# Performance work log

Hardware: AMD Instinct MI355X
Metric: run time of the kernel (lower is better)

Reference implementation:

```python
import jax, jax.numpy as jnp
import numpy as np

N_NODES = 50000
N_EDGES = 800000
N_GRAPHS = 512
IN_CH, HID_CH, OUT_CH, N_CLASSES = 128, 64, 64, 10


def gcn_conv(x, src, dst, ew, W, b, n_nodes):
    """PyG GCNConv: add self-loops (weight 1), symmetric normalization, x @ W, scatter-add at dst, + bias."""
    xw = x @ W  # [N, out]
    loop = jnp.arange(n_nodes, dtype=src.dtype)
    src_f = jnp.concatenate([src, loop])
    dst_f = jnp.concatenate([dst, loop])
    ew_f = jnp.concatenate([ew, jnp.ones((n_nodes,), dtype=ew.dtype)])
    deg = jax.ops.segment_sum(ew_f, dst_f, num_segments=n_nodes)  # [N]
    dinv = jnp.where(deg > 0, jax.lax.rsqrt(deg), 0.0)
    norm = dinv[src_f] * ew_f * dinv[dst_f]  # [E+N]
    msg = norm[:, None] * xw[src_f]  # gather + scale
    out = jax.ops.segment_sum(msg, dst_f, num_segments=n_nodes)  # scatter-add
    return out + b


def setup_inputs() -> dict:
    key = jax.random.key(0)
    ks = jax.random.split(key, 12)
    x = jax.random.normal(ks[0], (N_NODES, IN_CH), dtype=jnp.float32)
    edge_index = jax.random.randint(ks[1], (2, N_EDGES), 0, N_NODES, dtype=jnp.int64)
    edge_attr = jax.random.uniform(ks[2], (N_EDGES,), dtype=jnp.float32)
    batch = jnp.sort(jax.random.randint(ks[3], (N_NODES,), 0, N_GRAPHS, dtype=jnp.int64))
    def glorot(k, shape):
        lim = np.sqrt(6.0 / (shape[0] + shape[1]))
        return jax.random.uniform(k, shape, jnp.float32, -lim, lim)
    W1 = glorot(ks[4], (IN_CH, HID_CH))
    b1 = jnp.zeros((HID_CH,), jnp.float32)
    W2 = glorot(ks[5], (HID_CH, OUT_CH))
    b2 = jnp.zeros((OUT_CH,), jnp.float32)
    LW1 = glorot(ks[6], (OUT_CH, 32))
    Lb1 = jnp.zeros((32,), jnp.float32)
    LW2 = glorot(ks[7], (32, N_CLASSES))
    Lb2 = jnp.zeros((N_CLASSES,), jnp.float32)
    return {"x": x, "edge_index": edge_index, "edge_attr": edge_attr, "batch": batch,
            "W1": W1, "b1": b1, "W2": W2, "b2": b2,
            "LW1": LW1, "Lb1": Lb1, "LW2": LW2, "Lb2": Lb2}


def reference(x, edge_index, edge_attr, batch, W1, b1, W2, b2, LW1, Lb1, LW2, Lb2):
    src, dst = edge_index[0], edge_index[1]
    h = gcn_conv(x, src, dst, edge_attr, W1, b1, N_NODES)
    h = jax.nn.relu(h)
    h = gcn_conv(h, src, dst, edge_attr, W2, b2, N_NODES)
    # global mean pool over graphs
    sums = jax.ops.segment_sum(h, batch, num_segments=N_GRAPHS)  # [G, OUT]
    cnt = jax.ops.segment_sum(jnp.ones((N_NODES,), h.dtype), batch, num_segments=N_GRAPHS)
    pooled = sums / jnp.maximum(cnt, 1.0)[:, None]
    # head (dropout treated as identity for deterministic reference)
    h1 = pooled @ LW1 + Lb1
    return h1 @ LW2 + Lb2
```

## Files before the change

kernel.cpp:

```cpp
#include <hip/hip_runtime.h>
#include <hip/hip_bf16.h>

static constexpr int NN = 50000;
static constexpr int NE = 800000;
static constexpr int NG = 512;
static constexpr int NB = 196;


__global__ void zero_kernel(float* __restrict__ p, int n) {
    int i = blockIdx.x * blockDim.x + threadIdx.x;
    if (i < n) p[i] = 0.f;
}

__global__ void hist64_kernel(const int* __restrict__ dst, const float* __restrict__ ew,
                              unsigned long long* __restrict__ h, int* __restrict__ rank) {
    int e = blockIdx.x * blockDim.x + threadIdx.x;
    if (e >= NE) return;
    int d = dst[e];
    unsigned int fx = __float2uint_rn(ew[e] * 1048576.0f);
    unsigned long long pack = (1ULL << 40) | (unsigned long long)fx;
    unsigned long long old = atomicAdd(&h[d], pack);
    rank[e] = (int)(old >> 40);
}

__global__ void dinv_kernel(const unsigned long long* __restrict__ h,
                            float* __restrict__ dinv) {
    int i = blockIdx.x * blockDim.x + threadIdx.x;
    if (i < NN) {
        float deg = (float)(h[i] & ((1ULL << 40) - 1)) * (1.0f / 1048576.0f) + 1.0f;
        dinv[i] = 1.0f / sqrtf(deg);
    }
}


__device__ __forceinline__ int block_scan_inclusive(int v, int* wtot) {
    int lane = threadIdx.x & 63, wid = threadIdx.x >> 6;
    int inc = v;
#pragma unroll
    for (int off = 1; off < 64; off <<= 1) {
        int n = __shfl_up(inc, (unsigned)off, 64);
        if (lane >= off) inc += n;
    }
    if (lane == 63) wtot[wid] = inc;
    __syncthreads();
    int add = 0;
    for (int w = 0; w < wid; ++w) add += wtot[w];
    return inc + add;
}

__global__ __launch_bounds__(256) void scanA_kernel(const unsigned long long* __restrict__ h,
                                                    int* __restrict__ partial) {
    int i = blockIdx.x * 256 + threadIdx.x;
    int v = (i < NN) ? (int)(h[i] >> 40) : 0;
    __shared__ int wsum[4];
    int lane = threadIdx.x & 63, wid = threadIdx.x >> 6;
#pragma unroll
    for (int off = 32; off > 0; off >>= 1) v += __shfl_down(v, (unsigned)off, 64);
    if (lane == 0) wsum[wid] = v;
    __syncthreads();
    if (threadIdx.x == 0) partial[blockIdx.x] = wsum[0] + wsum[1] + wsum[2] + wsum[3];
}

__global__ __launch_bounds__(256) void scanB_kernel(const int* __restrict__ partial,
                                                    int* __restrict__ poff) {
    __shared__ int wtot[4];
    int t = threadIdx.x;
    int v = (t < NB) ? partial[t] : 0;
    int incl = block_scan_inclusive(v, wtot);
    if (t < NB) poff[t] = incl - v;
}

__global__ __launch_bounds__(256) void scanC_kernel(const unsigned long long* __restrict__ h,
                                                    const int* __restrict__ poff,
                                                    int* __restrict__ rowptr) {
    __shared__ int wtot[4];
    int i = blockIdx.x * 256 + threadIdx.x;
    int v = (i < NN) ? (int)(h[i] >> 40) : 0;
    int incl = block_scan_inclusive(v, wtot);
    if (i < NN) rowptr[i + 1] = poff[blockIdx.x] + incl;
    if (i == 0) rowptr[0] = 0;
}

__global__ void scatter_kernel(const int* __restrict__ src, const int* __restrict__ dst,
                               const float* __restrict__ ew, const float* __restrict__ dinv,
                               const int* __restrict__ rowptr, const int* __restrict__ rank,
                               int2* __restrict__ epack) {
    int e = blockIdx.x * blockDim.x + threadIdx.x;
    if (e >= NE) return;
    int s = src[e], d = dst[e];
    int pos = rowptr[d] + rank[e];
    float coef = dinv[s] * ew[e] * dinv[d];
    epack[pos] = make_int2(s, __float_as_int(coef));
}

__global__ void bounds_kernel(const int* __restrict__ batch, int* __restrict__ gbeg,
                              int* __restrict__ gend) {
    int i = blockIdx.x * blockDim.x + threadIdx.x;
    if (i >= NN) return;
    int g = batch[i];
    if (i == 0 || batch[i - 1] != g) gbeg[g] = i;
    if (i == NN - 1 || batch[i + 1] != g) gend[g] = i + 1;
}

template <int K>
__global__ __launch_bounds__(256) void gemm_kernel(const float* __restrict__ X,
                                                   const float* __restrict__ W,
                                                   ushort* __restrict__ out) {
    __shared__ float Xs[64][68];
    __shared__ float Ws[K][64];
    for (int i = threadIdx.x; i < K * 16; i += 256)
        ((float4*)Ws)[i] = ((const float4*)W)[i];
    int tx = threadIdx.x & 15, ty = threadIdx.x >> 4;
    int row0 = blockIdx.x * 64;
    float acc[4][4] = {};
    for (int kb = 0; kb < K; kb += 64) {
        __syncthreads();
        for (int i = threadIdx.x; i < 1024; i += 256) {
            int r = i >> 4, k4 = i & 15;
            int gr = row0 + r; if (gr >= NN) gr = NN - 1;
            float4 v = *(const float4*)(X + (long long)gr * K + kb + k4 * 4);
            *(float4*)&Xs[r][k4 * 4] = v;
        }
        __syncthreads();
#pragma unroll 16
        for (int k = 0; k < 64; ++k) {
            float4 wv = *(const float4*)&Ws[kb + k][tx * 4];
            float x0 = Xs[ty * 4 + 0][k];
            float x1 = Xs[ty * 4 + 1][k];
            float x2 = Xs[ty * 4 + 2][k];
            float x3 = Xs[ty * 4 + 3][k];
            acc[0][0] = fmaf(x0, wv.x, acc[0][0]); acc[0][1] = fmaf(x0, wv.y, acc[0][1]);
            acc[0][2] = fmaf(x0, wv.z, acc[0][2]); acc[0][3] = fmaf(x0, wv.w, acc[0][3]);
            acc[1][0] = fmaf(x1, wv.x, acc[1][0]); acc[1][1] = fmaf(x1, wv.y, acc[1][1]);
            acc[1][2] = fmaf(x1, wv.z, acc[1][2]); acc[1][3] = fmaf(x1, wv.w, acc[1][3]);
            acc[2][0] = fmaf(x2, wv.x, acc[2][0]); acc[2][1] = fmaf(x2, wv.y, acc[2][1]);
            acc[2][2] = fmaf(x2, wv.z, acc[2][2]); acc[2][3] = fmaf(x2, wv.w, acc[2][3]);
            acc[3][0] = fmaf(x3, wv.x, acc[3][0]); acc[3][1] = fmaf(x3, wv.y, acc[3][1]);
            acc[3][2] = fmaf(x3, wv.z, acc[3][2]); acc[3][3] = fmaf(x3, wv.w, acc[3][3]);
        }
    }
#pragma unroll
    for (int j = 0; j < 4; ++j) {
        int r = row0 + ty * 4 + j;
        if (r < NN) {
            ushort4 sv;
            sv.x = __hip_bfloat16_raw(__float2bfloat16(acc[j][0])).x;
            sv.y = __hip_bfloat16_raw(__float2bfloat16(acc[j][1])).x;
            sv.z = __hip_bfloat16_raw(__float2bfloat16(acc[j][2])).x;
            sv.w = __hip_bfloat16_raw(__float2bfloat16(acc[j][3])).x;
            *(ushort4*)(out + (long long)r * 64 + tx * 4) = sv;
        }
    }
}

__device__ __forceinline__ float bf16_ld(const ushort* p) {
    return __uint_as_float((unsigned)(*p) << 16);
}

template <bool RELU>
__global__ __launch_bounds__(256) void agg_kernel(const ushort* __restrict__ xw,
                                                  const int* __restrict__ rowptr,
                                                  const int2* __restrict__ epack,
                                                  const float* __restrict__ dinv,
                                                  const float* __restrict__ bias,
                                                  float* __restrict__ out) {
    int node = blockIdx.x * 4 + (threadIdx.x >> 6);
    int c = threadIdx.x & 63;
    if (node >= NN) return;
    float di = dinv[node];
    float acc = fmaf(di * di, bf16_ld(xw + node * 64 + c), bias[c]);
    float acc2 = 0.f;
    int j = rowptr[node], end = rowptr[node + 1];
    for (; j + 3 < end; j += 4) {
        int2 p0 = epack[j];
        int2 p1 = epack[j + 1];
        int2 p2 = epack[j + 2];
        int2 p3 = epack[j + 3];
        float v0 = bf16_ld(xw + p0.x * 64 + c);
        float v1 = bf16_ld(xw + p1.x * 64 + c);
        float v2 = bf16_ld(xw + p2.x * 64 + c);
        float v3 = bf16_ld(xw + p3.x * 64 + c);
        acc  = fmaf(__int_as_float(p0.y), v0, acc);
        acc2 = fmaf(__int_as_float(p1.y), v1, acc2);
        acc  = fmaf(__int_as_float(p2.y), v2, acc);
        acc2 = fmaf(__int_as_float(p3.y), v3, acc2);
    }
    for (; j < end; ++j) {
        int2 p0 = epack[j];
        acc = fmaf(__int_as_float(p0.y), bf16_ld(xw + p0.x * 64 + c), acc);
    }
    acc += acc2;
    if (RELU) acc = fmaxf(acc, 0.f);
    out[node * 64 + c] = acc;
}

__global__ __launch_bounds__(256) void poolhead_kernel(const float* __restrict__ h,
                                                       const int* __restrict__ gbeg,
                                                       const int* __restrict__ gend,
                                                       const float* __restrict__ LW1,
                                                       const float* __restrict__ Lb1,
                                                       const float* __restrict__ LW2,
                                                       const float* __restrict__ Lb2,
                                                       float* __restrict__ out) {
    __shared__ float pp[4][64];
    __shared__ float p[64];
    __shared__ float t1[32];
    int g = blockIdx.x, t = threadIdx.x;
    int lane = t & 63, wid = t >> 6;
    int b = gbeg[g], e = gend[g];
    float acc = 0.f;
    for (int i = b + wid; i < e; i += 4) acc += h[i * 64 + lane];
    pp[wid][lane] = acc;
    __syncthreads();
    if (t < 64) {
        float s = pp[0][t] + pp[1][t] + pp[2][t] + pp[3][t];
        p[t] = s / fmaxf((float)(e - b), 1.0f);
    }
    __syncthreads();
    if (t < 32) {
        float a = Lb1[t];
#pragma unroll
        for (int k = 0; k < 64; ++k) a = fmaf(p[k], LW1[k * 32 + t], a);
        t1[t] = a;
    }
    __syncthreads();
    if (t < 10) {
        float a = Lb2[t];
#pragma unroll
        for (int j = 0; j < 32; ++j) a = fmaf(t1[j], LW2[j * 10 + t], a);
        out[g * 10 + t] = a;
    }
}


extern "C" void kernel_launch(void* const* d_in, const int* in_sizes, int n_in,
                              void* d_out, int out_size, void* d_ws, size_t ws_size,
                              hipStream_t stream) {
    const float* x     = (const float*)d_in[0];
    const int*   ei    = (const int*)d_in[1];
    const float* ew    = (const float*)d_in[2];
    const int*   batch = (const int*)d_in[3];
    const float* W1    = (const float*)d_in[4];
    const float* b1    = (const float*)d_in[5];
    const float* W2    = (const float*)d_in[6];
    const float* b2    = (const float*)d_in[7];
    const float* LW1   = (const float*)d_in[8];
    const float* Lb1   = (const float*)d_in[9];
    const float* LW2   = (const float*)d_in[10];
    const float* Lb2   = (const float*)d_in[11];

    const int* src = ei;
    const int* dst = ei + NE;

    float* ws = (float*)d_ws;
    unsigned long long* h64 = (unsigned long long*)ws;
    int*   gbeg   = (int*)(ws + 100096);
    int*   gend   = (int*)(ws + 100608);
    float* dinv   = ws + 101120;
    int*   rowptr = (int*)(ws + 151168);
    int*   partial  = (int*)(ws + 201216);
    int*   poff     = (int*)(ws + 201472);
    int2*  epack  = (int2*)(ws + 201728);
    ushort* bufA  = (ushort*)(ws + 1801728);
    float* bufB   = ws + 5001728;
    int*   rank   = (int*)(ws + 5001728);

    zero_kernel<<<(101120 + 255) / 256, 256, 0, stream>>>(ws, 101120);

    hist64_kernel<<<(NE + 255) / 256, 256, 0, stream>>>(dst, ew, h64, rank);
    dinv_kernel<<<NB, 256, 0, stream>>>(h64, dinv);
    scanA_kernel<<<NB, 256, 0, stream>>>(h64, partial);
    scanB_kernel<<<1, 256, 0, stream>>>(partial, poff);
    scanC_kernel<<<NB, 256, 0, stream>>>(h64, poff, rowptr);
    scatter_kernel<<<(NE + 255) / 256, 256, 0, stream>>>(src, dst, ew, dinv, rowptr, rank, epack);
    bounds_kernel<<<NB, 256, 0, stream>>>(batch, gbeg, gend);

    gemm_kernel<128><<<(NN + 63) / 64, 256, 0, stream>>>(x, W1, bufA);
    agg_kernel<true><<<(NN + 3) / 4, 256, 0, stream>>>(bufA, rowptr, epack, dinv, b1, bufB);

    gemm_kernel<64><<<(NN + 63) / 64, 256, 0, stream>>>(bufB, W2, bufA);
    agg_kernel<false><<<(NN + 3) / 4, 256, 0, stream>>>(bufA, rowptr, epack, dinv, b2, bufB);

    poolhead_kernel<<<NG, 256, 0, stream>>>(bufB, gbeg, gend, LW1, Lb1, LW2, Lb2, (float*)d_out);
}
```

Measured before the change: 275.9 us.

## Fuse setup kernels, store hidden layer in bf16, vectorize aggregation across edge halves

Merges the dinv and scanA kernels, and folds the graph-bounds computation into scanC, cutting two launches. The hidden activation after layer 1 is now stored as bf16, and the second GEMM gets a bf16-input load path, halving that intermediate's traffic. The aggregation kernel now has each lane handle two channels via ushort2 loads, with the two half-waves processing alternating edges and combining through a shuffle. The dst-side dinv factor moves out of the per-edge coefficient into a single multiply per node. The extra bf16 rounding of the hidden layer adds precision loss, and half the lanes sit idle during the output writes.

```diff
diff --git a/kernel.cpp b/kernel.cpp
--- a/kernel.cpp
+++ b/kernel.cpp
@@ -5,6 +5,13 @@
 static constexpr int NE = 800000;
 static constexpr int NG = 512;
 static constexpr int NB = 196;
+
+__device__ __forceinline__ float bfu(ushort u) {
+    return __uint_as_float((unsigned)u << 16);
+}
+__device__ __forceinline__ ushort fbf(float f) {
+    return __hip_bfloat16_raw(__float2bfloat16(f)).x;
+}
 
 
 __global__ void zero_kernel(float* __restrict__ p, int n) {
@@ -23,15 +30,26 @@
     rank[e] = (int)(old >> 40);
 }
 
-__global__ void dinv_kernel(const unsigned long long* __restrict__ h,
-                            float* __restrict__ dinv) {
-    int i = blockIdx.x * blockDim.x + threadIdx.x;
+__global__ __launch_bounds__(256) void dinv_scanA_kernel(const unsigned long long* __restrict__ h,
+                                                         float* __restrict__ dinv,
+                                                         int* __restrict__ partial) {
+    int i = blockIdx.x * 256 + threadIdx.x;
+    int cnt = 0;
     if (i < NN) {
-        float deg = (float)(h[i] & ((1ULL << 40) - 1)) * (1.0f / 1048576.0f) + 1.0f;
+        unsigned long long v = h[i];
+        cnt = (int)(v >> 40);
+        float deg = (float)(v & ((1ULL << 40) - 1)) * (1.0f / 1048576.0f) + 1.0f;
         dinv[i] = 1.0f / sqrtf(deg);
     }
-}
-
+    __shared__ int wsum[4];
+    int lane = threadIdx.x & 63, wid = threadIdx.x >> 6;
+    int v = cnt;
+#pragma unroll
+    for (int off = 32; off > 0; off >>= 1) v += __shfl_down(v, (unsigned)off, 64);
+    if (lane == 0) wsum[wid] = v;
+    __syncthreads();
+    if (threadIdx.x == 0) partial[blockIdx.x] = wsum[0] + wsum[1] + wsum[2] + wsum[3];
+}
 
 __device__ __forceinline__ int block_scan_inclusive(int v, int* wtot) {
     int lane = threadIdx.x & 63, wid = threadIdx.x >> 6;
@@ -46,19 +64,6 @@
     int add = 0;
     for (int w = 0; w < wid; ++w) add += wtot[w];
     return inc + add;
-}
-
-__global__ __launch_bounds__(256) void scanA_kernel(const unsigned long long* __restrict__ h,
-                                                    int* __restrict__ partial) {
-    int i = blockIdx.x * 256 + threadIdx.x;
-    int v = (i < NN) ? (int)(h[i] >> 40) : 0;
-    __shared__ int wsum[4];
-    int lane = threadIdx.x & 63, wid = threadIdx.x >> 6;
-#pragma unroll
-    for (int off = 32; off > 0; off >>= 1) v += __shfl_down(v, (unsigned)off, 64);
-    if (lane == 0) wsum[wid] = v;
-    __syncthreads();
-    if (threadIdx.x == 0) partial[blockIdx.x] = wsum[0] + wsum[1] + wsum[2] + wsum[3];
 }
 
 __global__ __launch_bounds__(256) void scanB_kernel(const int* __restrict__ partial,
@@ -70,14 +75,22 @@
     if (t < NB) poff[t] = incl - v;
 }
 
-__global__ __launch_bounds__(256) void scanC_kernel(const unsigned long long* __restrict__ h,
-                                                    const int* __restrict__ poff,
-                                                    int* __restrict__ rowptr) {
+__global__ __launch_bounds__(256) void scanC_bounds_kernel(const unsigned long long* __restrict__ h,
+                                                           const int* __restrict__ poff,
+                                                           int* __restrict__ rowptr,
+                                                           const int* __restrict__ batch,
+                                                           int* __restrict__ gbeg,
+                                                           int* __restrict__ gend) {
     __shared__ int wtot[4];
     int i = blockIdx.x * 256 + threadIdx.x;
     int v = (i < NN) ? (int)(h[i] >> 40) : 0;
     int incl = block_scan_inclusive(v, wtot);
-    if (i < NN) rowptr[i + 1] = poff[blockIdx.x] + incl;
+    if (i < NN) {
+        rowptr[i + 1] = poff[blockIdx.x] + incl;
+        int g = batch[i];
+        if (i == 0 || batch[i - 1] != g) gbeg[g] = i;
+        if (i == NN - 1 || batch[i + 1] != g) gend[g] = i + 1;
+    }
     if (i == 0) rowptr[0] = 0;
 }
 
@@ -89,21 +102,12 @@
     if (e >= NE) return;
     int s = src[e], d = dst[e];
     int pos = rowptr[d] + rank[e];
-    float coef = dinv[s] * ew[e] * dinv[d];
+    float coef = dinv[s] * ew[e];
     epack[pos] = make_int2(s, __float_as_int(coef));
 }
 
-__global__ void bounds_kernel(const int* __restrict__ batch, int* __restrict__ gbeg,
-                              int* __restrict__ gend) {
-    int i = blockIdx.x * blockDim.x + threadIdx.x;
-    if (i >= NN) return;
-    int g = batch[i];
-    if (i == 0 || batch[i - 1] != g) gbeg[g] = i;
-    if (i == NN - 1 || batch[i + 1] != g) gend[g] = i + 1;
-}
-
-template <int K>
-__global__ __launch_bounds__(256) void gemm_kernel(const float* __restrict__ X,
+template <int K, bool BF16IN>
+__global__ __launch_bounds__(256) void gemm_kernel(const void* __restrict__ Xv,
                                                    const float* __restrict__ W,
                                                    ushort* __restrict__ out) {
     __shared__ float Xs[64][68];
@@ -115,11 +119,28 @@
     float acc[4][4] = {};
     for (int kb = 0; kb < K; kb += 64) {
         __syncthreads();
-        for (int i = threadIdx.x; i < 1024; i += 256) {
-            int r = i >> 4, k4 = i & 15;
-            int gr = row0 + r; if (gr >= NN) gr = NN - 1;
-            float4 v = *(const float4*)(X + (long long)gr * K + kb + k4 * 4);
-            *(float4*)&Xs[r][k4 * 4] = v;
+        if constexpr (BF16IN) {
+            const ushort* X = (const ushort*)Xv;
+            for (int i = threadIdx.x; i < 512; i += 256) {
+                int r = i >> 3, g = i & 7;
+                int gr = row0 + r; if (gr >= NN) gr = NN - 1;
+                uint4 v = *(const uint4*)(X + (long long)gr * K + kb + g * 8);
+                float4 f0, f1;
+                f0.x = __uint_as_float(v.x << 16); f0.y = __uint_as_float(v.x & 0xffff0000u);
+                f0.z = __uint_as_float(v.y << 16); f0.w = __uint_as_float(v.y & 0xffff0000u);
+                f1.x = __uint_as_float(v.z << 16); f1.y = __uint_as_float(v.z & 0xffff0000u);
+                f1.z = __uint_as_float(v.w << 16); f1.w = __uint_as_float(v.w & 0xffff0000u);
+                *(float4*)&Xs[r][g * 8] = f0;
+                *(float4*)&Xs[r][g * 8 + 4] = f1;
+            }
+        } else {
+            const float* X = (const float*)Xv;
+            for (int i = threadIdx.x; i < 1024; i += 256) {
+                int r = i >> 4, k4 = i & 15;
+                int gr = row0 + r; if (gr >= NN) gr = NN - 1;
+                float4 v = *(const float4*)(X + (long long)gr * K + kb + k4 * 4);
+                *(float4*)&Xs[r][k4 * 4] = v;
+            }
         }
         __syncthreads();
 #pragma unroll 16
@@ -144,54 +165,65 @@
         int r = row0 + ty * 4 + j;
         if (r < NN) {
             ushort4 sv;
-            sv.x = __hip_bfloat16_raw(__float2bfloat16(acc[j][0])).x;
-            sv.y = __hip_bfloat16_raw(__float2bfloat16(acc[j][1])).x;
-            sv.z = __hip_bfloat16_raw(__float2bfloat16(acc[j][2])).x;
-            sv.w = __hip_bfloat16_raw(__float2bfloat16(acc[j][3])).x;
+            sv.x = fbf(acc[j][0]); sv.y = fbf(acc[j][1]);
+            sv.z = fbf(acc[j][2]); sv.w = fbf(acc[j][3]);
             *(ushort4*)(out + (long long)r * 64 + tx * 4) = sv;
         }
     }
 }
 
-__device__ __forceinline__ float bf16_ld(const ushort* p) {
-    return __uint_as_float((unsigned)(*p) << 16);
-}
-
-template <bool RELU>
+template <bool RELU, typename OutT>
 __global__ __launch_bounds__(256) void agg_kernel(const ushort* __restrict__ xw,
                                                   const int* __restrict__ rowptr,
                                                   const int2* __restrict__ epack,
                                                   const float* __restrict__ dinv,
                                                   const float* __restrict__ bias,
-                                                  float* __restrict__ out) {
+                                                  OutT* __restrict__ out) {
     int node = blockIdx.x * 4 + (threadIdx.x >> 6);
-    int c = threadIdx.x & 63;
     if (node >= NN) return;
-    float di = dinv[node];
-    float acc = fmaf(di * di, bf16_ld(xw + node * 64 + c), bias[c]);
-    float acc2 = 0.f;
-    int j = rowptr[node], end = rowptr[node + 1];
-    for (; j + 3 < end; j += 4) {
-        int2 p0 = epack[j];
-        int2 p1 = epack[j + 1];
-        int2 p2 = epack[j + 2];
-        int2 p3 = epack[j + 3];
-        float v0 = bf16_ld(xw + p0.x * 64 + c);
-        float v1 = bf16_ld(xw + p1.x * 64 + c);
-        float v2 = bf16_ld(xw + p2.x * 64 + c);
-        float v3 = bf16_ld(xw + p3.x * 64 + c);
-        acc  = fmaf(__int_as_float(p0.y), v0, acc);
-        acc2 = fmaf(__int_as_float(p1.y), v1, acc2);
-        acc  = fmaf(__int_as_float(p2.y), v2, acc);
-        acc2 = fmaf(__int_as_float(p3.y), v3, acc2);
-    }
-    for (; j < end; ++j) {
-        int2 p0 = epack[j];
-        acc = fmaf(__int_as_float(p0.y), bf16_ld(xw + p0.x * 64 + c), acc);
-    }
-    acc += acc2;
-    if (RELU) acc = fmaxf(acc, 0.f);
-    out[node * 64 + c] = acc;
+    int lane = threadIdx.x & 63;
+    int half = lane >> 5;
+    int c2 = lane & 31;
+    int beg = rowptr[node], end = rowptr[node + 1];
+    float a0 = 0.f, a1 = 0.f, b0 = 0.f, b1 = 0.f;
+    int j = beg + half;
+    for (; j + 2 < end; j += 4) {
+        int2 pa = epack[j];
+        int2 pb = epack[j + 2];
+        ushort2 ua = *(const ushort2*)(xw + pa.x * 64 + 2 * c2);
+        ushort2 ub = *(const ushort2*)(xw + pb.x * 64 + 2 * c2);
+        float wa = __int_as_float(pa.y);
+        float wb = __int_as_float(pb.y);
+        a0 = fmaf(wa, bfu(ua.x), a0);
+        a1 = fmaf(wa, bfu(ua.y), a1);
+        b0 = fmaf(wb, bfu(ub.x), b0);
+        b1 = fmaf(wb, bfu(ub.y), b1);
+    }
+    if (j < end) {
+        int2 pa = epack[j];
+        ushort2 ua = *(const ushort2*)(xw + pa.x * 64 + 2 * c2);
+        float wa = __int_as_float(pa.y);
+        a0 = fmaf(wa, bfu(ua.x), a0);
+        a1 = fmaf(wa, bfu(ua.y), a1);
+    }
+    a0 += b0; a1 += b1;
+    a0 += __shfl_xor(a0, 32);
+    a1 += __shfl_xor(a1, 32);
+    if (half == 0) {
+        float di = dinv[node];
+        ushort2 us = *(const ushort2*)(xw + node * 64 + 2 * c2);
+        float2 bv = *(const float2*)(bias + 2 * c2);
+        float o0 = fmaf(di, a0, fmaf(di * di, bfu(us.x), bv.x));
+        float o1 = fmaf(di, a1, fmaf(di * di, bfu(us.y), bv.y));
+        if (RELU) { o0 = fmaxf(o0, 0.f); o1 = fmaxf(o1, 0.f); }
+        if constexpr (sizeof(OutT) == 2) {
+            ushort2 sv; sv.x = fbf(o0); sv.y = fbf(o1);
+            *(ushort2*)((ushort*)out + node * 64 + 2 * c2) = sv;
+        } else {
+            float2 fv; fv.x = o0; fv.y = o1;
+            *(float2*)((float*)out + node * 64 + 2 * c2) = fv;
+        }
+    }
 }
 
 __global__ __launch_bounds__(256) void poolhead_kernel(const float* __restrict__ h,
@@ -258,28 +290,27 @@
     int*   gend   = (int*)(ws + 100608);
     float* dinv   = ws + 101120;
     int*   rowptr = (int*)(ws + 151168);
-    int*   partial  = (int*)(ws + 201216);
-    int*   poff     = (int*)(ws + 201472);
+    int*   partial= (int*)(ws + 201216);
+    int*   poff   = (int*)(ws + 201472);
     int2*  epack  = (int2*)(ws + 201728);
-    ushort* bufA  = (ushort*)(ws + 1801728);
-    float* bufB   = ws + 5001728;
-    int*   rank   = (int*)(ws + 5001728);
+    ushort* xwA   = (ushort*)(ws + 1801728);
+    ushort* h1    = (ushort*)(ws + 3401728);
+    float* h2     = ws + 3401728;
+    int*   rank   = (int*)(ws + 6601728);
 
     zero_kernel<<<(101120 + 255) / 256, 256, 0, stream>>>(ws, 101120);
 
     hist64_kernel<<<(NE + 255) / 256, 256, 0, stream>>>(dst, ew, h64, rank);
-    dinv_kernel<<<NB, 256, 0, stream>>>(h64, dinv);
-    scanA_kernel<<<NB, 256, 0, stream>>>(h64, partial);
+    dinv_scanA_kernel<<<NB, 256, 0, stream>>>(h64, dinv, partial);
     scanB_kernel<<<1, 256, 0, stream>>>(partial, poff);
-    scanC_kernel<<<NB, 256, 0, stream>>>(h64, poff, rowptr);
+    scanC_bounds_kernel<<<NB, 256, 0, stream>>>(h64, poff, rowptr, batch, gbeg, gend);
     scatter_kernel<<<(NE + 255) / 256, 256, 0, stream>>>(src, dst, ew, dinv, rowptr, rank, epack);
-    bounds_kernel<<<NB, 256, 0, stream>>>(batch, gbeg, gend);
-
-    gemm_kernel<128><<<(NN + 63) / 64, 256, 0, stream>>>(x, W1, bufA);
-    agg_kernel<true><<<(NN + 3) / 4, 256, 0, stream>>>(bufA, rowptr, epack, dinv, b1, bufB);
-
-    gemm_kernel<64><<<(NN + 63) / 64, 256, 0, stream>>>(bufB, W2, bufA);
-    agg_kernel<false><<<(NN + 3) / 4, 256, 0, stream>>>(bufA, rowptr, epack, dinv, b2, bufB);
-
-    poolhead_kernel<<<NG, 256, 0, stream>>>(bufB, gbeg, gend, LW1, Lb1, LW2, Lb2, (float*)d_out);
-}
+
+    gemm_kernel<128, false><<<(NN + 63) / 64, 256, 0, stream>>>(x, W1, xwA);
+    agg_kernel<true, ushort><<<(NN + 3) / 4, 256, 0, stream>>>(xwA, rowptr, epack, dinv, b1, h1);
+
+    gemm_kernel<64, true><<<(NN + 63) / 64, 256, 0, stream>>>(h1, W2, xwA);
+    agg_kernel<false, float><<<(NN + 3) / 4, 256, 0, stream>>>(xwA, rowptr, epack, dinv, b2, h2);
+
+    poolhead_kernel<<<NG, 256, 0, stream>>>(h2, gbeg, gend, LW1, Lb1, LW2, Lb2, (float*)d_out);
+}
```

Measured after the change: 264.1 us. 1.04x faster.
